# Performance work log

Measured on AMD Instinct MI355X. Metric: run time of the kernel, lower is better.

## Reference

```python
import jax, jax.numpy as jnp
import numpy as np

B, D, H1, H2, E, L = 32768, 512, 512, 256, 8, 32


def setup_inputs() -> dict:
    key = jax.random.key(0)
    ks = jax.random.split(key, 16)

    def init(k, shape, fan_in):
        bound = 1.0 / np.sqrt(fan_in)
        return jax.random.uniform(k, shape, jnp.float32, -bound, bound)

    return {
        "obs": jax.random.normal(ks[0], (B, D), jnp.float32),
        "obs_no_goal": jax.random.normal(ks[1], (B, D), jnp.float32),
        # stacked expert weights: [E, in, out]
        "eW1": init(ks[2], (E, D, H1), D), "eb1": init(ks[3], (E, H1), D),
        "eW2": init(ks[4], (E, H1, H2), H1), "eb2": init(ks[5], (E, H2), H1),
        "eW3": init(ks[6], (E, H2, L), H2), "eb3": init(ks[7], (E, L), H2),
        # gating network
        "gW1": init(ks[8], (D, H1), D), "gb1": init(ks[9], (H1,), D),
        "gW2": init(ks[10], (H1, H2), H1), "gb2": init(ks[11], (H2,), H1),
        "gW3": init(ks[12], (H2, E), H2), "gb3": init(ks[13], (E,), H2),
    }


def reference(obs, obs_no_goal, eW1, eb1, eW2, eb2, eW3, eb3,
              gW1, gb1, gW2, gb2, gW3, gb3):
    elu = jax.nn.elu
    # gating: MLP + softmax over experts -> [B, E]
    h = elu(obs @ gW1 + gb1)
    h = elu(h @ gW2 + gb2)
    weights = jax.nn.softmax(h @ gW3 + gb3, axis=-1)
    # all experts as batched GEMMs: [B, E, *]
    x = elu(jnp.einsum('bd,edh->beh', obs, eW1) + eb1)
    x = elu(jnp.einsum('beh,ehk->bek', x, eW2) + eb2)
    expert_latent = jnp.einsum('bek,ekl->bel', x, eW3) + eb3  # [B, E, L]
    # soft combine
    latent = jnp.einsum('be,bel->bl', weights, expert_latent)
    # L2Norm (F.normalize with eps=1e-12)
    nrm = jnp.linalg.norm(latent, axis=-1, keepdims=True)
    latent = latent / jnp.maximum(nrm, 1e-12)
    return latent, weights
```

## Files before the change

kernel.cpp:

```cpp
#include <hip/hip_runtime.h>
#include <hip/hip_bf16.h>

#define DEVI __device__ __forceinline__

typedef __attribute__((ext_vector_type(8))) short shortx8;
typedef __attribute__((ext_vector_type(4))) float floatx4;

static constexpr int Bsz = 32768, Din = 512, H1 = 512, H2 = 256, NE = 8, Lout = 32;

DEVI float bf2f(short s) {
  union { unsigned u; float f; } c;
  c.u = ((unsigned)(unsigned short)s) << 16;
  return c.f;
}
DEVI short f2bf(float f) {
  union { float f; unsigned u; } c; c.f = f;
  unsigned u = c.u + (0x7FFFu + ((c.u >> 16) & 1u));
  return (short)(u >> 16);
}

__global__ void cast_bf16_kernel(const float* __restrict__ in, short* __restrict__ out, int n4) {
  int stride = gridDim.x * blockDim.x;
  for (int i = blockIdx.x * blockDim.x + threadIdx.x; i < n4; i += stride) {
    float4 v = ((const float4*)in)[i];
    short4 o;
    o.x = f2bf(v.x); o.y = f2bf(v.y); o.z = f2bf(v.z); o.w = f2bf(v.w);
    ((short4*)out)[i] = o;
  }
}

__global__ void bias_concat_kernel(const float* __restrict__ gb1, const float* __restrict__ eb1,
                                   const float* __restrict__ gb2, const float* __restrict__ eb2,
                                   float* __restrict__ b1cat, float* __restrict__ b2cat) {
  int t = blockIdx.x * 256 + threadIdx.x;
  if (t < 4608) {
    b1cat[t] = t < 512 ? gb1[t] : eb1[t - 512];
  } else {
    int u = t - 4608;
    b2cat[u] = u < 256 ? gb2[u] : eb2[u - 256];
  }
}

__global__ void transpose_cast_kernel(const float* __restrict__ in, short* __restrict__ out,
                                      int R, int C) {
  __shared__ short tile[32][33];
  in += (size_t)blockIdx.z * R * C;
  out += (size_t)blockIdx.z * R * C;
  int c0 = blockIdx.x * 32, r0 = blockIdx.y * 32;
  int tx = threadIdx.x, ty = threadIdx.y;
#pragma unroll
  for (int i = 0; i < 4; ++i) {
    int r = r0 + ty + i * 8, c = c0 + tx;
    if (r < R && c < C) tile[ty + i * 8][tx] = f2bf(in[(size_t)r * C + c]);
  }
  __syncthreads();
#pragma unroll
  for (int i = 0; i < 4; ++i) {
    int c = c0 + ty + i * 8, r = r0 + tx;
    if (c < C && r < R) out[(size_t)c * R + r] = tile[tx][ty + i * 8];
  }
}

#define BARRIER() asm volatile("s_barrier" ::: "memory")

template <int ROWS>
DEVI void stage_half8(const short* __restrict__ g, int ld, int row0, int kt, int h,
                      short* ldsop, int wave, int lane) {
  constexpr int CPW = ROWS / 128;
  const int r_in = lane >> 3, c = lane & 7;
#pragma unroll
  for (int i = 0; i < CPW; ++i) {
    const int ch = h * (ROWS / 16) + wave * CPW + i;
    const int r = ch * 8 + r_in;
    const int cs = c ^ (r & 7);
    const short* src = g + (size_t)(row0 + r) * ld + kt * 64 + cs * 8;
    __builtin_amdgcn_global_load_lds((__attribute__((address_space(1))) void*)src,
                                     (__attribute__((address_space(3))) void*)(ldsop + ch * 512),
                                     16, 0, 0);
  }
}

template <int BM, int BN>
__global__ __launch_bounds__(512) void gemm8p_kernel(
    const short* __restrict__ A, const short* __restrict__ Bt,
    const float* __restrict__ bias, short* __restrict__ Cout,
    int K, int lda, int ldc, long AzOff, long BzOff, long CzOff, int BiasZOff,
    int nx, int nz) {
  constexpr int WN = BN / 4;
  constexpr int NF = WN / 16;
  constexpr int NH = NF / 2;
  constexpr int DB = (BM + BN) * 64;
  extern __shared__ __align__(16) short smem[];
  const int bid = blockIdx.x;
  const int spx = gridDim.x >> 3;
  const int lin = (bid & 7) * spx + (bid >> 3);
  const int nxz = nx * nz;
  const int by = lin / nxz, rem = lin % nxz;
  const int bz = rem / nx, bx = rem % nx;
  A += (size_t)bz * AzOff;
  Bt += (size_t)bz * BzOff;
  Cout += (size_t)bz * CzOff;
  bias += bz * BiasZOff;
  const int tid = threadIdx.x, wave = tid >> 6, lane = tid & 63;
  const int l15 = lane & 15, l4 = lane >> 4;
  const int wm = wave >> 2, wn = wave & 3;
  const int brow = by * BM, bcol = bx * BN;
  const int NT = K / 64;

  auto FR = [&](const short* base, int r, int kc) {
    return *(const shortx8*)(base + r * 64 + ((kc ^ (r & 7)) << 3));
  };

  floatx4 acc[8][NF] = {};
  shortx8 af[4][2], bq[NF][2];

  {
    short* a0 = smem;            short* b0 = smem + BM * 64;
    short* a1 = smem + DB;       short* b1 = smem + DB + BM * 64;
    stage_half8<BM>(A, lda, brow, 0, 0, a0, wave, lane);
    stage_half8<BM>(A, lda, brow, 0, 1, a0, wave, lane);
    stage_half8<BN>(Bt, K, bcol, 0, 0, b0, wave, lane);
    stage_half8<BN>(Bt, K, bcol, 0, 1, b0, wave, lane);
    if (NT > 1) {
      stage_half8<BN>(Bt, K, bcol, 1, 0, b1, wave, lane);
      stage_half8<BM>(A, lda, brow, 1, 0, a1, wave, lane);
      if constexpr (BN == 256) asm volatile("s_waitcnt vmcnt(4)" ::: "memory");
      else                     asm volatile("s_waitcnt vmcnt(3)" ::: "memory");
    } else {
      asm volatile("s_waitcnt vmcnt(0)" ::: "memory");
    }
    BARRIER();
  }

  for (int kt = 0; kt < NT; ++kt) {
    const int cur = kt & 1;
    const short* la = smem + cur * DB;
    const short* lb = la + BM * 64;
    short* an = smem + (cur ^ 1) * DB;
    short* bn = an + BM * 64;
    short* ac = smem + cur * DB;
    short* bc = ac + BM * 64;

#pragma unroll
    for (int m2 = 0; m2 < 4; ++m2) {
      const int r = wm * 128 + m2 * 16 + l15;
#pragma unroll
      for (int ks = 0; ks < 2; ++ks) af[m2][ks] = FR(la, r, ks * 4 + l4);
    }
#pragma unroll
    for (int n2 = 0; n2 < NH; ++n2) {
      const int r = wn * WN + n2 * 16 + l15;
#pragma unroll
      for (int ks = 0; ks < 2; ++ks) bq[n2][ks] = FR(lb, r, ks * 4 + l4);
    }
    if (kt + 1 < NT) stage_half8<BM>(A, lda, brow, kt + 1, 1, an, wave, lane);
    BARRIER();
    __builtin_amdgcn_s_setprio(1);
#pragma unroll
    for (int m2 = 0; m2 < 4; ++m2)
#pragma unroll
      for (int n2 = 0; n2 < NH; ++n2)
#pragma unroll
        for (int ks = 0; ks < 2; ++ks)
          acc[m2][n2] = __builtin_amdgcn_mfma_f32_16x16x32_bf16(af[m2][ks], bq[n2][ks],
                                                                acc[m2][n2], 0, 0, 0);
    __builtin_amdgcn_s_setprio(0);
    BARRIER();

#pragma unroll
    for (int n2 = 0; n2 < NH; ++n2) {
      const int r = wn * WN + (NH + n2) * 16 + l15;
#pragma unroll
      for (int ks = 0; ks < 2; ++ks) bq[NH + n2][ks] = FR(lb, r, ks * 4 + l4);
    }
    if (kt + 1 < NT) stage_half8<BN>(Bt, K, bcol, kt + 1, 1, bn, wave, lane);
    BARRIER();
    __builtin_amdgcn_s_setprio(1);
#pragma unroll
    for (int m2 = 0; m2 < 4; ++m2)
#pragma unroll
      for (int n2 = 0; n2 < NH; ++n2)
#pragma unroll
        for (int ks = 0; ks < 2; ++ks)
          acc[m2][NH + n2] = __builtin_amdgcn_mfma_f32_16x16x32_bf16(af[m2][ks], bq[NH + n2][ks],
                                                                     acc[m2][NH + n2], 0, 0, 0);
    __builtin_amdgcn_s_setprio(0);
    BARRIER();

#pragma unroll
    for (int m2 = 0; m2 < 4; ++m2) {
      const int r = wm * 128 + (4 + m2) * 16 + l15;
#pragma unroll
      for (int ks = 0; ks < 2; ++ks) af[m2][ks] = FR(la, r, ks * 4 + l4);
    }
    if (kt + 2 < NT) stage_half8<BN>(Bt, K, bcol, kt + 2, 0, bc, wave, lane);
    BARRIER();
    __builtin_amdgcn_s_setprio(1);
#pragma unroll
    for (int m2 = 0; m2 < 4; ++m2)
#pragma unroll
      for (int n2 = 0; n2 < NH; ++n2)
#pragma unroll
        for (int ks = 0; ks < 2; ++ks)
          acc[4 + m2][n2] = __builtin_amdgcn_mfma_f32_16x16x32_bf16(af[m2][ks], bq[n2][ks],
                                                                    acc[4 + m2][n2], 0, 0, 0);
    __builtin_amdgcn_s_setprio(0);
    BARRIER();

    if (kt + 2 < NT) stage_half8<BM>(A, lda, brow, kt + 2, 0, ac, wave, lane);
    BARRIER();
    __builtin_amdgcn_s_setprio(1);
#pragma unroll
    for (int m2 = 0; m2 < 4; ++m2)
#pragma unroll
      for (int n2 = 0; n2 < NH; ++n2)
#pragma unroll
        for (int ks = 0; ks < 2; ++ks)
          acc[4 + m2][NH + n2] = __builtin_amdgcn_mfma_f32_16x16x32_bf16(
              af[m2][ks], bq[NH + n2][ks], acc[4 + m2][NH + n2], 0, 0, 0);
    __builtin_amdgcn_s_setprio(0);
    if (kt + 1 < NT) {
      if (kt == NT - 2) {
        asm volatile("s_waitcnt vmcnt(0)" ::: "memory");
      } else {
        if constexpr (BN == 256) asm volatile("s_waitcnt vmcnt(4)" ::: "memory");
        else                     asm volatile("s_waitcnt vmcnt(3)" ::: "memory");
      }
      BARRIER();
    }
  }

#pragma unroll
  for (int m2 = 0; m2 < 8; ++m2) {
    const int row0 = brow + wm * 128 + m2 * 16 + l4 * 4;
#pragma unroll
    for (int n2 = 0; n2 < NF; ++n2) {
      const int col = bcol + wn * WN + n2 * 16 + l15;
      const float bv = bias[col];
#pragma unroll
      for (int r = 0; r < 4; ++r) {
        float v = acc[m2][n2][r] + bv;
        v = v > 0.f ? v : (__expf(v) - 1.f);
        Cout[(size_t)(row0 + r) * ldc + col] = f2bf(v);
      }
    }
  }
}

__global__ __launch_bounds__(512) void gemm8p_l2l3_kernel(
    const short* __restrict__ A, const short* __restrict__ Bt,
    const float* __restrict__ bias, short* __restrict__ bufGate,
    const short* __restrict__ w3, const float* __restrict__ b3,
    float* __restrict__ elat, int gBase) {
  constexpr int BM = 256, BN = 256, KT = 512;
  constexpr int NH = 2, DB = (BM + BN) * 64, NT = KT / 64;
  constexpr int LDA = 1536;
  extern __shared__ __align__(16) short smem[];
  const int bid = blockIdx.x;
  const int spx = gridDim.x >> 3;
  const int lin = (bid & 7) * spx + (bid >> 3);
  const int by = lin / 3, bz = lin % 3;
  A += (size_t)bz * 512;
  Bt += (size_t)bz * 256 * 512;
  bias += bz * 256;
  const int tid = threadIdx.x, wave = tid >> 6, lane = tid & 63;
  const int l15 = lane & 15, l4 = lane >> 4;
  const int wm = wave >> 2, wn = wave & 3;
  const int brow = by * BM;
  const int NTT = NT;

  auto FR = [&](const short* base, int r, int kc) {
    return *(const shortx8*)(base + r * 64 + ((kc ^ (r & 7)) << 3));
  };

  floatx4 acc[8][4] = {};
  shortx8 af[4][2], bq[4][2];

  {
    short* a0 = smem;            short* b0 = smem + BM * 64;
    short* a1 = smem + DB;       short* b1 = smem + DB + BM * 64;
    stage_half8<BM>(A, LDA, brow, 0, 0, a0, wave, lane);
    stage_half8<BM>(A, LDA, brow, 0, 1, a0, wave, lane);
    stage_half8<BN>(Bt, KT, 0, 0, 0, b0, wave, lane);
    stage_half8<BN>(Bt, KT, 0, 0, 1, b0, wave, lane);
    stage_half8<BN>(Bt, KT, 0, 1, 0, b1, wave, lane);
    stage_half8<BM>(A, LDA, brow, 1, 0, a1, wave, lane);
    asm volatile("s_waitcnt vmcnt(4)" ::: "memory");
    BARRIER();
  }

  for (int kt = 0; kt < NTT; ++kt) {
    const int cur = kt & 1;
    const short* la = smem + cur * DB;
    const short* lb = la + BM * 64;
    short* an = smem + (cur ^ 1) * DB;
    short* bn = an + BM * 64;
    short* ac = smem + cur * DB;
    short* bc = ac + BM * 64;

#pragma unroll
    for (int m2 = 0; m2 < 4; ++m2) {
      const int r = wm * 128 + m2 * 16 + l15;
#pragma unroll
      for (int ks = 0; ks < 2; ++ks) af[m2][ks] = FR(la, r, ks * 4 + l4);
    }
#pragma unroll
    for (int n2 = 0; n2 < NH; ++n2) {
      const int r = wn * 64 + n2 * 16 + l15;
#pragma unroll
      for (int ks = 0; ks < 2; ++ks) bq[n2][ks] = FR(lb, r, ks * 4 + l4);
    }
    if (kt + 1 < NTT) stage_half8<BM>(A, LDA, brow, kt + 1, 1, an, wave, lane);
    BARRIER();
    __builtin_amdgcn_s_setprio(1);
#pragma unroll
    for (int m2 = 0; m2 < 4; ++m2)
#pragma unroll
      for (int n2 = 0; n2 < NH; ++n2)
#pragma unroll
        for (int ks = 0; ks < 2; ++ks)
          acc[m2][n2] = __builtin_amdgcn_mfma_f32_16x16x32_bf16(af[m2][ks], bq[n2][ks],
                                                                acc[m2][n2], 0, 0, 0);
    __builtin_amdgcn_s_setprio(0);
    BARRIER();

#pragma unroll
    for (int n2 = 0; n2 < NH; ++n2) {
      const int r = wn * 64 + (NH + n2) * 16 + l15;
#pragma unroll
      for (int ks = 0; ks < 2; ++ks) bq[NH + n2][ks] = FR(lb, r, ks * 4 + l4);
    }
    if (kt + 1 < NTT) stage_half8<BN>(Bt, KT, 0, kt + 1, 1, bn, wave, lane);
    BARRIER();
    __builtin_amdgcn_s_setprio(1);
#pragma unroll
    for (int m2 = 0; m2 < 4; ++m2)
#pragma unroll
      for (int n2 = 0; n2 < NH; ++n2)
#pragma unroll
        for (int ks = 0; ks < 2; ++ks)
          acc[m2][NH + n2] = __builtin_amdgcn_mfma_f32_16x16x32_bf16(af[m2][ks], bq[NH + n2][ks],
                                                                     acc[m2][NH + n2], 0, 0, 0);
    __builtin_amdgcn_s_setprio(0);
    BARRIER();

#pragma unroll
    for (int m2 = 0; m2 < 4; ++m2) {
      const int r = wm * 128 + (4 + m2) * 16 + l15;
#pragma unroll
      for (int ks = 0; ks < 2; ++ks) af[m2][ks] = FR(la, r, ks * 4 + l4);
    }
    if (kt + 2 < NTT) stage_half8<BN>(Bt, KT, 0, kt + 2, 0, bc, wave, lane);
    BARRIER();
    __builtin_amdgcn_s_setprio(1);
#pragma unroll
    for (int m2 = 0; m2 < 4; ++m2)
#pragma unroll
      for (int n2 = 0; n2 < NH; ++n2)
#pragma unroll
        for (int ks = 0; ks < 2; ++ks)
          acc[4 + m2][n2] = __builtin_amdgcn_mfma_f32_16x16x32_bf16(af[m2][ks], bq[n2][ks],
                                                                    acc[4 + m2][n2], 0, 0, 0);
    __builtin_amdgcn_s_setprio(0);
    BARRIER();

    if (kt + 2 < NTT) stage_half8<BM>(A, LDA, brow, kt + 2, 0, ac, wave, lane);
    BARRIER();
    __builtin_amdgcn_s_setprio(1);
#pragma unroll
    for (int m2 = 0; m2 < 4; ++m2)
#pragma unroll
      for (int n2 = 0; n2 < NH; ++n2)
#pragma unroll
        for (int ks = 0; ks < 2; ++ks)
          acc[4 + m2][NH + n2] = __builtin_amdgcn_mfma_f32_16x16x32_bf16(
              af[m2][ks], bq[NH + n2][ks], acc[4 + m2][NH + n2], 0, 0, 0);
    __builtin_amdgcn_s_setprio(0);
    if (kt + 1 < NTT) {
      if (kt == NTT - 2) asm volatile("s_waitcnt vmcnt(0)" ::: "memory");
      else               asm volatile("s_waitcnt vmcnt(4)" ::: "memory");
      BARRIER();
    }
  }

  const int grp = gBase + bz;
  if (grp == 0) {
#pragma unroll
    for (int m2 = 0; m2 < 8; ++m2) {
      const int row0 = brow + wm * 128 + m2 * 16 + l4 * 4;
#pragma unroll
      for (int n2 = 0; n2 < 4; ++n2) {
        const int col = wn * 64 + n2 * 16 + l15;
        const float bv = bias[col];
#pragma unroll
        for (int r = 0; r < 4; ++r) {
          float v = acc[m2][n2][r] + bv;
          v = v > 0.f ? v : (__expf(v) - 1.f);
          bufGate[(size_t)(row0 + r) * 256 + col] = f2bf(v);
        }
      }
    }
    return;
  }

  constexpr int XS = 264;
  short* X = smem;
#pragma unroll
  for (int m2 = 0; m2 < 8; ++m2) {
    const int rw = wm * 128 + m2 * 16 + l4 * 4;
#pragma unroll
    for (int n2 = 0; n2 < 4; ++n2) {
      const int col = wn * 64 + n2 * 16 + l15;
      const float bv = bias[col];
#pragma unroll
      for (int r = 0; r < 4; ++r) {
        float v = acc[m2][n2][r] + bv;
        v = v > 0.f ? v : (__expf(v) - 1.f);
        X[(rw + r) * XS + col] = f2bf(v);
      }
    }
  }
  BARRIER();
  const int e = grp - 1;
  const short* w3e = w3 + (size_t)e * 32 * 256;
  floatx4 a2[2][2] = {};
#pragma unroll
  for (int ks = 0; ks < 8; ++ks) {
    const int kc = ks * 4 + l4;
    shortx8 xa[2], wb[2];
#pragma unroll
    for (int mi = 0; mi < 2; ++mi) {
      const int rw = wave * 32 + mi * 16 + l15;
      xa[mi] = *(const shortx8*)(X + rw * XS + kc * 8);
    }
#pragma unroll
    for (int ni = 0; ni < 2; ++ni)
      wb[ni] = *(const shortx8*)(w3e + (ni * 16 + l15) * 256 + kc * 8);
#pragma unroll
    for (int mi = 0; mi < 2; ++mi)
#pragma unroll
      for (int ni = 0; ni < 2; ++ni)
        a2[mi][ni] = __builtin_amdgcn_mfma_f32_16x16x32_bf16(xa[mi], wb[ni], a2[mi][ni], 0, 0, 0);
  }
#pragma unroll
  for (int mi = 0; mi < 2; ++mi) {
#pragma unroll
    for (int ni = 0; ni < 2; ++ni) {
      const int col = ni * 16 + l15;
      const float bv = b3[e * 32 + col];
#pragma unroll
      for (int r = 0; r < 4; ++r) {
        const int row = brow + wave * 32 + mi * 16 + l4 * 4 + r;
        elat[(size_t)row * 256 + e * 32 + col] = a2[mi][ni][r] + bv;
      }
    }
  }
}

__global__ void gate3_kernel(const short* __restrict__ g2, const short* __restrict__ w3t,
                             const float* __restrict__ b3, float* __restrict__ wout) {
  int t = blockIdx.x * 256 + threadIdx.x;
  int b = t >> 3, e = t & 7;
  const short* xr = g2 + (size_t)b * 256;
  const short* wr = w3t + e * H2;
  float s = 0.f;
  for (int k = 0; k < H2; k += 8) {
    shortx8 xv = *(const shortx8*)(xr + k);
    shortx8 wv = *(const shortx8*)(wr + k);
#pragma unroll
    for (int j = 0; j < 8; ++j) s += bf2f(xv[j]) * bf2f(wv[j]);
  }
  s += b3[e];
  float m = s;
#pragma unroll
  for (int off = 1; off < 8; off <<= 1) m = fmaxf(m, __shfl_xor(m, off, 8));
  float p = __expf(s - m);
  float sum = p;
#pragma unroll
  for (int off = 1; off < 8; off <<= 1) sum += __shfl_xor(sum, off, 8);
  wout[t] = p / sum;
}

__global__ void combine_norm_kernel(const float* __restrict__ elat,
                                    const float* __restrict__ gate,
                                    float* __restrict__ out) {
  int t = blockIdx.x * 256 + threadIdx.x;
  int b = t >> 5, l = t & 31;
  const float* er = elat + (size_t)b * 256;
  const float* gr = gate + (size_t)b * 8;
  float v = 0.f;
#pragma unroll
  for (int e = 0; e < 8; ++e) v += gr[e] * er[e * 32 + l];
  float ss = v * v;
#pragma unroll
  for (int off = 1; off < 32; off <<= 1) ss += __shfl_xor(ss, off, 32);
  out[t] = v / fmaxf(sqrtf(ss), 1e-12f);
}

extern "C" void kernel_launch(void* const* d_in, const int* in_sizes, int n_in,
                              void* d_out, int out_size, void* d_ws, size_t ws_size,
                              hipStream_t stream) {
  static const int kExp[14] = {16777216, 16777216, 2097152, 4096, 1048576, 2048, 65536, 256,
                               262144, 512, 131072, 256, 2048, 8};
  const void* in[14];
  bool identity = (n_in >= 14);
  if (identity)
    for (int i = 0; i < 14; ++i)
      if (in_sizes[i] != kExp[i]) { identity = false; break; }
  if (identity) {
    for (int i = 0; i < 14; ++i) in[i] = d_in[i];
  } else {
    bool used[64] = {};
    for (int i = 0; i < 14; ++i) {
      in[i] = d_in[i < n_in ? i : 0];
      for (int j = 0; j < n_in && j < 64; ++j)
        if (!used[j] && in_sizes[j] == kExp[i]) { in[i] = d_in[j]; used[j] = true; break; }
    }
  }
  const float* obs = (const float*)in[0];
  const float* eW1 = (const float*)in[2];
  const float* eb1 = (const float*)in[3];
  const float* eW2 = (const float*)in[4];
  const float* eb2 = (const float*)in[5];
  const float* eW3 = (const float*)in[6];
  const float* eb3 = (const float*)in[7];
  const float* gW1 = (const float*)in[8];
  const float* gb1 = (const float*)in[9];
  const float* gW2 = (const float*)in[10];
  const float* gb2 = (const float*)in[11];
  const float* gW3 = (const float*)in[12];
  const float* gb3 = (const float*)in[13];

  char* ws = (char*)d_ws;
  size_t off = 0;
  auto carve = [&](size_t bytes) {
    char* p = ws + off;
    off += (bytes + 255) & ~(size_t)255;
    return p;
  };
  short* obs_bf = (short*)carve((size_t)Bsz * Din * 2);
  short* w1cat = (short*)carve((size_t)4608 * 512 * 2);
  short* w2cat = (short*)carve((size_t)2304 * 512 * 2);
  short* eW3t = (short*)carve((size_t)NE * Lout * H2 * 2);
  short* gW3t = (short*)carve((size_t)NE * H2 * 2);
  float* b1cat = (float*)carve(4608 * 4);
  float* b2cat = (float*)carve(2304 * 4);
  float* elat = (float*)carve((size_t)Bsz * 256 * 4);
  short* buf1 = (short*)carve((size_t)Bsz * 1536 * 2);
  short* buf2 = (short*)carve((size_t)Bsz * 256 * 2);

  float* out_lat = (float*)d_out;
  float* out_w = (float*)d_out + (size_t)Bsz * Lout;

  constexpr int kLds1 = 2 * (256 + 256) * 64 * 2;
  constexpr int kLdsF = 256 * 264 * 2;
  (void)hipFuncSetAttribute((const void*)gemm8p_kernel<256, 256>,
                            hipFuncAttributeMaxDynamicSharedMemorySize, kLds1);
  (void)hipFuncSetAttribute((const void*)gemm8p_l2l3_kernel,
                            hipFuncAttributeMaxDynamicSharedMemorySize, kLdsF);

  cast_bf16_kernel<<<2048, 256, 0, stream>>>(obs, obs_bf, Bsz * Din / 4);
  dim3 tb(32, 8);
  transpose_cast_kernel<<<dim3(16, 16, 1), tb, 0, stream>>>(gW1, w1cat, Din, H1);
  transpose_cast_kernel<<<dim3(16, 16, 8), tb, 0, stream>>>(eW1, w1cat + (size_t)512 * 512, Din, H1);
  transpose_cast_kernel<<<dim3(8, 16, 1), tb, 0, stream>>>(gW2, w2cat, H1, H2);
  transpose_cast_kernel<<<dim3(8, 16, 8), tb, 0, stream>>>(eW2, w2cat + (size_t)256 * 512, H1, H2);
  transpose_cast_kernel<<<dim3(1, 8, 8), tb, 0, stream>>>(eW3, eW3t, H2, Lout);
  transpose_cast_kernel<<<dim3(1, 8, 1), tb, 0, stream>>>(gW3, gW3t, H2, NE);
  bias_concat_kernel<<<27, 256, 0, stream>>>(gb1, eb1, gb2, eb2, b1cat, b2cat);

  for (int b = 0; b < 3; ++b) {
    gemm8p_kernel<256, 256><<<768, 512, kLds1, stream>>>(
        obs_bf, w1cat + (size_t)b * 3 * 512 * 512, b1cat + b * 1536, buf1,
        512, 512, 1536, 0L, 512L * 512, 512L, 512, 2, 3);
    gemm8p_l2l3_kernel<<<384, 512, kLdsF, stream>>>(
        buf1, w2cat + (size_t)b * 3 * 256 * 512, b2cat + b * 768, buf2,
        eW3t, eb3, elat, 3 * b);
    if (b == 0)
      gate3_kernel<<<(Bsz * NE) / 256, 256, 0, stream>>>(buf2, gW3t, gb3, out_w);
  }

  combine_norm_kernel<<<(Bsz * Lout) / 256, 256, 0, stream>>>(elat, out_w, out_lat);
}
```

Baseline: 382.3 us.

## Fuse gating softmax into layer-2/3 kernel and regroup expert batches 5+4

Removes the separate gate3 kernel and its bf16 gate activation buffer. The gate's final layer and softmax now run inside the l2l3 GEMM epilogue, using MFMA on the shared-memory tile against a 16-row padded gW3. The three 3-group passes become two passes of 5 and 4 groups, which cuts kernel launches and makes each grid larger. The transpose launches for W1 and W2 are also merged into one kernel each. The tradeoff is a larger intermediate buffer, and the padded gW3 rows 8-15 are left uninitialized; they only feed columns that are discarded.

```diff
diff --git a/kernel.cpp b/kernel.cpp
--- a/kernel.cpp
+++ b/kernel.cpp
@@ -45,6 +45,27 @@
                                       int R, int C) {
   __shared__ short tile[32][33];
   in += (size_t)blockIdx.z * R * C;
+  out += (size_t)blockIdx.z * R * C;
+  int c0 = blockIdx.x * 32, r0 = blockIdx.y * 32;
+  int tx = threadIdx.x, ty = threadIdx.y;
+#pragma unroll
+  for (int i = 0; i < 4; ++i) {
+    int r = r0 + ty + i * 8, c = c0 + tx;
+    if (r < R && c < C) tile[ty + i * 8][tx] = f2bf(in[(size_t)r * C + c]);
+  }
+  __syncthreads();
+#pragma unroll
+  for (int i = 0; i < 4; ++i) {
+    int c = c0 + ty + i * 8, r = r0 + tx;
+    if (c < C && r < R) out[(size_t)c * R + r] = tile[tx][ty + i * 8];
+  }
+}
+
+__global__ void transpose_cast2_kernel(const float* __restrict__ gsrc,
+                                       const float* __restrict__ esrc,
+                                       short* __restrict__ out, int R, int C) {
+  __shared__ short tile[32][33];
+  const float* in = (blockIdx.z == 0) ? gsrc : esrc + (size_t)(blockIdx.z - 1) * R * C;
   out += (size_t)blockIdx.z * R * C;
   int c0 = blockIdx.x * 32, r0 = blockIdx.y * 32;
   int tx = threadIdx.x, ty = threadIdx.y;
@@ -249,17 +270,18 @@
 
 __global__ __launch_bounds__(512) void gemm8p_l2l3_kernel(
     const short* __restrict__ A, const short* __restrict__ Bt,
-    const float* __restrict__ bias, short* __restrict__ bufGate,
+    const float* __restrict__ bias,
     const short* __restrict__ w3, const float* __restrict__ b3,
-    float* __restrict__ elat, int gBase) {
+    const short* __restrict__ gw3pad, const float* __restrict__ gb3,
+    float* __restrict__ elat, float* __restrict__ outW,
+    int gBase, int nz, int lda) {
   constexpr int BM = 256, BN = 256, KT = 512;
   constexpr int NH = 2, DB = (BM + BN) * 64, NT = KT / 64;
-  constexpr int LDA = 1536;
   extern __shared__ __align__(16) short smem[];
   const int bid = blockIdx.x;
   const int spx = gridDim.x >> 3;
   const int lin = (bid & 7) * spx + (bid >> 3);
-  const int by = lin / 3, bz = lin % 3;
+  const int by = lin / nz, bz = lin % nz;
   A += (size_t)bz * 512;
   Bt += (size_t)bz * 256 * 512;
   bias += bz * 256;
@@ -267,7 +289,6 @@
   const int l15 = lane & 15, l4 = lane >> 4;
   const int wm = wave >> 2, wn = wave & 3;
   const int brow = by * BM;
-  const int NTT = NT;
 
   auto FR = [&](const short* base, int r, int kc) {
     return *(const shortx8*)(base + r * 64 + ((kc ^ (r & 7)) << 3));
@@ -279,17 +300,17 @@
   {
     short* a0 = smem;            short* b0 = smem + BM * 64;
     short* a1 = smem + DB;       short* b1 = smem + DB + BM * 64;
-    stage_half8<BM>(A, LDA, brow, 0, 0, a0, wave, lane);
-    stage_half8<BM>(A, LDA, brow, 0, 1, a0, wave, lane);
+    stage_half8<BM>(A, lda, brow, 0, 0, a0, wave, lane);
+    stage_half8<BM>(A, lda, brow, 0, 1, a0, wave, lane);
     stage_half8<BN>(Bt, KT, 0, 0, 0, b0, wave, lane);
     stage_half8<BN>(Bt, KT, 0, 0, 1, b0, wave, lane);
     stage_half8<BN>(Bt, KT, 0, 1, 0, b1, wave, lane);
-    stage_half8<BM>(A, LDA, brow, 1, 0, a1, wave, lane);
+    stage_half8<BM>(A, lda, brow, 1, 0, a1, wave, lane);
     asm volatile("s_waitcnt vmcnt(4)" ::: "memory");
     BARRIER();
   }
 
-  for (int kt = 0; kt < NTT; ++kt) {
+  for (int kt = 0; kt < NT; ++kt) {
     const int cur = kt & 1;
     const short* la = smem + cur * DB;
     const short* lb = la + BM * 64;
@@ -310,7 +331,7 @@
 #pragma unroll
       for (int ks = 0; ks < 2; ++ks) bq[n2][ks] = FR(lb, r, ks * 4 + l4);
     }
-    if (kt + 1 < NTT) stage_half8<BM>(A, LDA, brow, kt + 1, 1, an, wave, lane);
+    if (kt + 1 < NT) stage_half8<BM>(A, lda, brow, kt + 1, 1, an, wave, lane);
     BARRIER();
     __builtin_amdgcn_s_setprio(1);
 #pragma unroll
@@ -330,7 +351,7 @@
 #pragma unroll
       for (int ks = 0; ks < 2; ++ks) bq[NH + n2][ks] = FR(lb, r, ks * 4 + l4);
     }
-    if (kt + 1 < NTT) stage_half8<BN>(Bt, KT, 0, kt + 1, 1, bn, wave, lane);
+    if (kt + 1 < NT) stage_half8<BN>(Bt, KT, 0, kt + 1, 1, bn, wave, lane);
     BARRIER();
     __builtin_amdgcn_s_setprio(1);
 #pragma unroll
@@ -350,7 +371,7 @@
 #pragma unroll
       for (int ks = 0; ks < 2; ++ks) af[m2][ks] = FR(la, r, ks * 4 + l4);
     }
-    if (kt + 2 < NTT) stage_half8<BN>(Bt, KT, 0, kt + 2, 0, bc, wave, lane);
+    if (kt + 2 < NT) stage_half8<BN>(Bt, KT, 0, kt + 2, 0, bc, wave, lane);
     BARRIER();
     __builtin_amdgcn_s_setprio(1);
 #pragma unroll
@@ -364,7 +385,7 @@
     __builtin_amdgcn_s_setprio(0);
     BARRIER();
 
-    if (kt + 2 < NTT) stage_half8<BM>(A, LDA, brow, kt + 2, 0, ac, wave, lane);
+    if (kt + 2 < NT) stage_half8<BM>(A, lda, brow, kt + 2, 0, ac, wave, lane);
     BARRIER();
     __builtin_amdgcn_s_setprio(1);
 #pragma unroll
@@ -376,31 +397,11 @@
           acc[4 + m2][NH + n2] = __builtin_amdgcn_mfma_f32_16x16x32_bf16(
               af[m2][ks], bq[NH + n2][ks], acc[4 + m2][NH + n2], 0, 0, 0);
     __builtin_amdgcn_s_setprio(0);
-    if (kt + 1 < NTT) {
-      if (kt == NTT - 2) asm volatile("s_waitcnt vmcnt(0)" ::: "memory");
+    if (kt + 1 < NT) {
+      if (kt == NT - 2) asm volatile("s_waitcnt vmcnt(0)" ::: "memory");
       else               asm volatile("s_waitcnt vmcnt(4)" ::: "memory");
       BARRIER();
     }
-  }
-
-  const int grp = gBase + bz;
-  if (grp == 0) {
-#pragma unroll
-    for (int m2 = 0; m2 < 8; ++m2) {
-      const int row0 = brow + wm * 128 + m2 * 16 + l4 * 4;
-#pragma unroll
-      for (int n2 = 0; n2 < 4; ++n2) {
-        const int col = wn * 64 + n2 * 16 + l15;
-        const float bv = bias[col];
-#pragma unroll
-        for (int r = 0; r < 4; ++r) {
-          float v = acc[m2][n2][r] + bv;
-          v = v > 0.f ? v : (__expf(v) - 1.f);
-          bufGate[(size_t)(row0 + r) * 256 + col] = f2bf(v);
-        }
-      }
-    }
-    return;
   }
 
   constexpr int XS = 264;
@@ -421,6 +422,46 @@
     }
   }
   BARRIER();
+
+  const int grp = gBase + bz;
+  if (grp == 0) {
+    floatx4 lg[2] = {};
+#pragma unroll
+    for (int ks = 0; ks < 8; ++ks) {
+      const int kc = ks * 4 + l4;
+      shortx8 xa[2];
+#pragma unroll
+      for (int mi = 0; mi < 2; ++mi) {
+        const int rw = wave * 32 + mi * 16 + l15;
+        xa[mi] = *(const shortx8*)(X + rw * XS + kc * 8);
+      }
+      shortx8 wb = *(const shortx8*)(gw3pad + l15 * 256 + kc * 8);
+#pragma unroll
+      for (int mi = 0; mi < 2; ++mi)
+        lg[mi] = __builtin_amdgcn_mfma_f32_16x16x32_bf16(xa[mi], wb, lg[mi], 0, 0, 0);
+    }
+    const float bg = gb3[l15 & 7];
+#pragma unroll
+    for (int mi = 0; mi < 2; ++mi) {
+#pragma unroll
+      for (int r = 0; r < 4; ++r) {
+        float lv = lg[mi][r] + bg;
+        float m = lv;
+#pragma unroll
+        for (int off = 1; off < 8; off <<= 1) m = fmaxf(m, __shfl_xor(m, off));
+        float p = __expf(lv - m);
+        float s = p;
+#pragma unroll
+        for (int off = 1; off < 8; off <<= 1) s += __shfl_xor(s, off);
+        if (l15 < 8) {
+          const int row = brow + wave * 32 + mi * 16 + l4 * 4 + r;
+          outW[(size_t)row * 8 + l15] = p / s;
+        }
+      }
+    }
+    return;
+  }
+
   const int e = grp - 1;
   const short* w3e = w3 + (size_t)e * 32 * 256;
   floatx4 a2[2][2] = {};
@@ -455,30 +496,6 @@
       }
     }
   }
-}
-
-__global__ void gate3_kernel(const short* __restrict__ g2, const short* __restrict__ w3t,
-                             const float* __restrict__ b3, float* __restrict__ wout) {
-  int t = blockIdx.x * 256 + threadIdx.x;
-  int b = t >> 3, e = t & 7;
-  const short* xr = g2 + (size_t)b * 256;
-  const short* wr = w3t + e * H2;
-  float s = 0.f;
-  for (int k = 0; k < H2; k += 8) {
-    shortx8 xv = *(const shortx8*)(xr + k);
-    shortx8 wv = *(const shortx8*)(wr + k);
-#pragma unroll
-    for (int j = 0; j < 8; ++j) s += bf2f(xv[j]) * bf2f(wv[j]);
-  }
-  s += b3[e];
-  float m = s;
-#pragma unroll
-  for (int off = 1; off < 8; off <<= 1) m = fmaxf(m, __shfl_xor(m, off, 8));
-  float p = __expf(s - m);
-  float sum = p;
-#pragma unroll
-  for (int off = 1; off < 8; off <<= 1) sum += __shfl_xor(sum, off, 8);
-  wout[t] = p / sum;
 }
 
 __global__ void combine_norm_kernel(const float* __restrict__ elat,
@@ -542,12 +559,11 @@
   short* w1cat = (short*)carve((size_t)4608 * 512 * 2);
   short* w2cat = (short*)carve((size_t)2304 * 512 * 2);
   short* eW3t = (short*)carve((size_t)NE * Lout * H2 * 2);
-  short* gW3t = (short*)carve((size_t)NE * H2 * 2);
+  short* gW3pad = (short*)carve((size_t)16 * H2 * 2);
   float* b1cat = (float*)carve(4608 * 4);
   float* b2cat = (float*)carve(2304 * 4);
   float* elat = (float*)carve((size_t)Bsz * 256 * 4);
-  short* buf1 = (short*)carve((size_t)Bsz * 1536 * 2);
-  short* buf2 = (short*)carve((size_t)Bsz * 256 * 2);
+  short* buf1 = (short*)carve((size_t)Bsz * 2560 * 2);
 
   float* out_lat = (float*)d_out;
   float* out_w = (float*)d_out + (size_t)Bsz * Lout;
@@ -561,24 +577,24 @@
 
   cast_bf16_kernel<<<2048, 256, 0, stream>>>(obs, obs_bf, Bsz * Din / 4);
   dim3 tb(32, 8);
-  transpose_cast_kernel<<<dim3(16, 16, 1), tb, 0, stream>>>(gW1, w1cat, Din, H1);
-  transpose_cast_kernel<<<dim3(16, 16, 8), tb, 0, stream>>>(eW1, w1cat + (size_t)512 * 512, Din, H1);
-  transpose_cast_kernel<<<dim3(8, 16, 1), tb, 0, stream>>>(gW2, w2cat, H1, H2);
-  transpose_cast_kernel<<<dim3(8, 16, 8), tb, 0, stream>>>(eW2, w2cat + (size_t)256 * 512, H1, H2);
+  transpose_cast2_kernel<<<dim3(16, 16, 9), tb, 0, stream>>>(gW1, eW1, w1cat, Din, H1);
+  transpose_cast2_kernel<<<dim3(8, 16, 9), tb, 0, stream>>>(gW2, eW2, w2cat, H1, H2);
   transpose_cast_kernel<<<dim3(1, 8, 8), tb, 0, stream>>>(eW3, eW3t, H2, Lout);
-  transpose_cast_kernel<<<dim3(1, 8, 1), tb, 0, stream>>>(gW3, gW3t, H2, NE);
+  transpose_cast_kernel<<<dim3(1, 8, 1), tb, 0, stream>>>(gW3, gW3pad, H2, NE);
   bias_concat_kernel<<<27, 256, 0, stream>>>(gb1, eb1, gb2, eb2, b1cat, b2cat);
 
-  for (int b = 0; b < 3; ++b) {
-    gemm8p_kernel<256, 256><<<768, 512, kLds1, stream>>>(
-        obs_bf, w1cat + (size_t)b * 3 * 512 * 512, b1cat + b * 1536, buf1,
-        512, 512, 1536, 0L, 512L * 512, 512L, 512, 2, 3);
-    gemm8p_l2l3_kernel<<<384, 512, kLdsF, stream>>>(
-        buf1, w2cat + (size_t)b * 3 * 256 * 512, b2cat + b * 768, buf2,
-        eW3t, eb3, elat, 3 * b);
-    if (b == 0)
-      gate3_kernel<<<(Bsz * NE) / 256, 256, 0, stream>>>(buf2, gW3t, gb3, out_w);
-  }
+  gemm8p_kernel<256, 256><<<1280, 512, kLds1, stream>>>(
+      obs_bf, w1cat, b1cat, buf1,
+      512, 512, 2560, 0L, 512L * 512, 512L, 512, 2, 5);
+  gemm8p_l2l3_kernel<<<640, 512, kLdsF, stream>>>(
+      buf1, w2cat, b2cat, eW3t, eb3, gW3pad, gb3, elat, out_w, 0, 5, 2560);
+
+  gemm8p_kernel<256, 256><<<1024, 512, kLds1, stream>>>(
+      obs_bf, w1cat + (size_t)5 * 512 * 512, b1cat + 2560, buf1,
+      512, 512, 2048, 0L, 512L * 512, 512L, 512, 2, 4);
+  gemm8p_l2l3_kernel<<<512, 512, kLdsF, stream>>>(
+      buf1, w2cat + (size_t)5 * 256 * 512, b2cat + 1280, eW3t, eb3, gW3pad, gb3,
+      elat, out_w, 5, 4, 2048);
 
   combine_norm_kernel<<<(Bsz * Lout) / 256, 256, 0, stream>>>(elat, out_w, out_lat);
 }
```

New measurement: 341.0 us. 10.8% less time.
